# Optimization experiments

Measured on AMD Instinct MI355X. Metric: run time of the kernel, lower is better.

Reference implementation:

```python
import jax, jax.numpy as jnp
import numpy as np

EMB_DIM = 1024
HEAD_NUM = 16
HEAD_DIM = EMB_DIM // HEAD_NUM
B, S = 2, 2048


def setup_inputs() -> dict:
    key = jax.random.key(0)
    k_x, k_wqkv, k_bqkv, k_wo, k_bo = jax.random.split(key, 5)
    x = jax.random.normal(k_x, (B, S, EMB_DIM), dtype=jnp.float32)
    # nn.Linear default init scale ~ 1/sqrt(fan_in); exact distribution irrelevant for a reference
    lim = 1.0 / np.sqrt(EMB_DIM)
    W_qkv = jax.random.uniform(k_wqkv, (EMB_DIM, 3 * EMB_DIM), jnp.float32, -lim, lim)
    b_qkv = jax.random.uniform(k_bqkv, (3 * EMB_DIM,), jnp.float32, -lim, lim)
    W_o = jax.random.uniform(k_wo, (EMB_DIM, EMB_DIM), jnp.float32, -lim, lim)
    b_o = jax.random.uniform(k_bo, (EMB_DIM,), jnp.float32, -lim, lim)
    mask = jnp.tril(jnp.ones((S, S), dtype=bool))  # causal mask as in casual_mask(seq_len)
    return {"x": x, "W_qkv": W_qkv, "b_qkv": b_qkv, "W_o": W_o, "b_o": b_o, "mask": mask}


def reference(x, W_qkv, b_qkv, W_o, b_o, mask):
    b, s, e = x.shape
    qkv = x @ W_qkv + b_qkv                      # [b, s, 3e]
    q, k, v = qkv[..., :e], qkv[..., e:2 * e], qkv[..., 2 * e:]
    # [b, s, h, d] -> [b, h, s, d]
    q = q.reshape(b, s, HEAD_NUM, HEAD_DIM).transpose(0, 2, 1, 3)
    k = k.reshape(b, s, HEAD_NUM, HEAD_DIM).transpose(0, 2, 1, 3)
    v = v.reshape(b, s, HEAD_NUM, HEAD_DIM).transpose(0, 2, 1, 3)
    scores = jnp.einsum("bhqd,bhkd->bhqk", q, k) / jnp.sqrt(jnp.float32(HEAD_DIM))
    scores = jnp.where(mask, scores, -jnp.inf)   # masked_fill(~mask, -inf)
    probs = jax.nn.softmax(scores, axis=-1)      # dropout is identity in eval mode
    out = jnp.einsum("bhqk,bhkd->bhqd", probs, v)
    out = out.transpose(0, 2, 1, 3).reshape(b, s, e)
    return out @ W_o + b_o
```

## Files before the change

### kernel.cpp

```cpp
#include <hip/hip_runtime.h>


typedef __attribute__((ext_vector_type(8))) short short8;
typedef __attribute__((ext_vector_type(4))) float floatx4;

#define NB 2
#define SEQ 2048
#define EMB 1024
#define NH 16
#define HD 64
#define M_ROWS (NB * SEQ)
#define N_QKV (3 * EMB)
#define SLOT_F 4160

#define GLL(g, l) __builtin_amdgcn_global_load_lds( \
    (const __attribute__((address_space(1))) void*)(g), \
    (__attribute__((address_space(3))) void*)(l), 16, 0, 0)

static __device__ __forceinline__ unsigned short f2bf(float f) {
    union { float f; unsigned int u; } v; v.f = f;
    unsigned int r = v.u + 0x7FFFu + ((v.u >> 16) & 1u);
    return (unsigned short)(r >> 16);
}

__global__ void x_to_bf16(const float* __restrict__ in, unsigned short* __restrict__ out, int n4) {
    int i = blockIdx.x * blockDim.x + threadIdx.x;
    if (i >= n4) return;
    float4 v = ((const float4*)in)[i];
    unsigned long long p = (unsigned long long)f2bf(v.x)
        | ((unsigned long long)f2bf(v.y) << 16)
        | ((unsigned long long)f2bf(v.z) << 32)
        | ((unsigned long long)f2bf(v.w) << 48);
    ((unsigned long long*)out)[i] = p;
}

__global__ void transpose_f32_bf16(const float* __restrict__ in,
                                   unsigned short* __restrict__ out, int R, int C) {
    __shared__ unsigned short tile[32][33];
    int tx = threadIdx.x, ty = threadIdx.y;
    int c0 = blockIdx.x * 32, r0 = blockIdx.y * 32;
    #pragma unroll
    for (int j = 0; j < 4; ++j)
        tile[ty + j * 8][tx] = f2bf(in[(size_t)(r0 + ty + j * 8) * C + c0 + tx]);
    __syncthreads();
    #pragma unroll
    for (int j = 0; j < 4; ++j)
        out[(size_t)(c0 + ty + j * 8) * R + r0 + tx] = tile[tx][ty + j * 8];
}

__global__ __launch_bounds__(256) void qkv_gemm(
    const unsigned short* __restrict__ A,
    const unsigned short* __restrict__ Bt,
    const float* __restrict__ bias,
    unsigned short* __restrict__ qb, unsigned short* __restrict__ kb,
    unsigned short* __restrict__ vb)
{
    const int K = EMB;
    __shared__ __align__(16) unsigned short As[128 * 32];
    __shared__ __align__(16) unsigned short Bs[128 * 32];
    int t = threadIdx.x;
    int m0 = blockIdx.y * 128;
    int n0 = blockIdx.x * 128;
    int w = t >> 6, lane = t & 63, quad = lane >> 4, lcol = lane & 15;
    int wr = w >> 1, wc = w & 1;

    floatx4 zero = {0.f, 0.f, 0.f, 0.f};
    floatx4 acc[4][4];
    #pragma unroll
    for (int i = 0; i < 4; ++i)
        #pragma unroll
        for (int j = 0; j < 4; ++j) acc[i][j] = zero;

    const unsigned short* a0 = A  + (size_t)(m0 + (t >> 2)) * K + ((t & 3) << 3);
    const unsigned short* b0 = Bt + (size_t)(n0 + (t >> 2)) * K + ((t & 3) << 3);
    unsigned short* la = &As[t << 3];
    unsigned short* lb = &Bs[t << 3];

    for (int k0 = 0; k0 < K; k0 += 32) {
        __syncthreads();
        GLL(a0 + k0, la);
        GLL(a0 + 64 * K + k0, la + 2048);
        GLL(b0 + k0, lb);
        GLL(b0 + 64 * K + k0, lb + 2048);
        __syncthreads();
        short8 af[4], bfm[4];
        #pragma unroll
        for (int i = 0; i < 4; ++i)
            af[i] = *(const short8*)(&As[(wr * 64 + i * 16 + lcol) * 32 + quad * 8]);
        #pragma unroll
        for (int j = 0; j < 4; ++j)
            bfm[j] = *(const short8*)(&Bs[(wc * 64 + j * 16 + lcol) * 32 + quad * 8]);
        #pragma unroll
        for (int i = 0; i < 4; ++i)
            #pragma unroll
            for (int j = 0; j < 4; ++j)
                acc[i][j] = __builtin_amdgcn_mfma_f32_16x16x32_bf16(af[i], bfm[j], acc[i][j], 0, 0, 0);
    }

    #pragma unroll
    for (int i = 0; i < 4; ++i) {
        int m = m0 + wr * 64 + i * 16 + quad * 4;
        int b = m >> 11, s = m & 2047;
        #pragma unroll
        for (int j = 0; j < 4; ++j) {
            int n = n0 + wc * 64 + j * 16 + lcol;
            int which = n >> 10;
            int e = n & 1023;
            int h = e >> 6, d = e & 63;
            float bv = bias[n];
            if (which == 2) {
                size_t base = ((size_t)((b * NH + h) * HD + d)) * SEQ + s;
                unsigned long long pk = (unsigned long long)f2bf(acc[i][j][0] + bv)
                    | ((unsigned long long)f2bf(acc[i][j][1] + bv) << 16)
                    | ((unsigned long long)f2bf(acc[i][j][2] + bv) << 32)
                    | ((unsigned long long)f2bf(acc[i][j][3] + bv) << 48);
                *(unsigned long long*)(&vb[base]) = pk;
            } else {
                unsigned short* dst = (which == 0) ? qb : kb;
                size_t base = ((size_t)((b * NH + h) * SEQ + s)) * HD + d;
                #pragma unroll
                for (int r = 0; r < 4; ++r)
                    dst[base + (size_t)r * HD] = f2bf(acc[i][j][r] + bv);
            }
        }
    }
}

#define PST 68

__global__ __launch_bounds__(256) void attn_partial(
    const unsigned short* __restrict__ Q,
    const unsigned short* __restrict__ Kk,
    const unsigned short* __restrict__ Vt,
    unsigned short* __restrict__ Out,
    float* __restrict__ Part)
{
    __shared__ __align__(16) unsigned short Ks[2][64 * 64];
    __shared__ __align__(16) unsigned short Vs[2][64 * 64];
    __shared__ __align__(16) unsigned short Ps[4][16 * PST];

    int u = blockIdx.x;
    int bh = blockIdx.y;
    int qt, c;
    if (u < 16) { qt = u; c = 0; }
    else { int v = u - 16; qt = 16 + (v >> 1); c = v & 1; }
    int ktBeg = c << 4;
    int ktEnd = (c == 0 && qt >= 16) ? 16 : (qt + 1);

    int q0 = qt * 64;
    int t = threadIdx.x;
    int w = t >> 6, lane = t & 63, quad = lane >> 4, lcol = lane & 15;
    const size_t hoff = (size_t)bh * SEQ * HD;
    const float SC = 0.18033688011112043f;

    const unsigned short* qp = Q + hoff + (size_t)(q0 + 16 * w + lcol) * HD + quad * 8;
    short8 aq0 = *(const short8*)qp, aq1 = *(const short8*)(qp + 32);

    int srow = t >> 3;
    int ss   = (t & 7) ^ (srow & 7);
    const unsigned short* kgl = Kk + hoff + (size_t)srow * HD + ss * 8;
    const unsigned short* vgl = Vt + hoff + (size_t)srow * SEQ + ss * 8;
    unsigned short* kld = &Ks[0][t * 8];
    unsigned short* vld = &Vs[0][t * 8];

    floatx4 zero = {0.f, 0.f, 0.f, 0.f};
    floatx4 O[4];
    float l[4] = {0.f, 0.f, 0.f, 0.f};
    #pragma unroll
    for (int d = 0; d < 4; ++d) O[d] = zero;

    {
        int k0 = ktBeg * 64;
        GLL(kgl + (size_t)k0 * HD, kld);
        GLL(kgl + (size_t)(k0 + 32) * HD, kld + 2048);
        GLL(vgl + k0, vld);
        GLL(vgl + (size_t)32 * SEQ + k0, vld + 2048);
    }

    int sx0 = (quad ^ (lcol & 7)) << 3;
    int sx1 = sx0 ^ 32;

    for (int kt = ktBeg; kt < ktEnd; ++kt) {
        int cur = kt & 1, nxt = cur ^ 1;
        __syncthreads();
        if (kt + 1 < ktEnd) {
            int k0 = (kt + 1) * 64;
            GLL(kgl + (size_t)k0 * HD, kld + nxt * 4096);
            GLL(kgl + (size_t)(k0 + 32) * HD, kld + nxt * 4096 + 2048);
            GLL(vgl + k0, vld + nxt * 4096);
            GLL(vgl + (size_t)32 * SEQ + k0, vld + nxt * 4096 + 2048);
        }

        const unsigned short* ksr = &Ks[cur][0];
        const unsigned short* vsr = &Vs[cur][0];
        short8 bk0[4], bk1[4], bv0[4], bv1[4];
        #pragma unroll
        for (int tc = 0; tc < 4; ++tc) {
            int rb = (tc * 16 + lcol) << 6;
            bk0[tc] = *(const short8*)(ksr + rb + sx0);
            bk1[tc] = *(const short8*)(ksr + rb + sx1);
            bv0[tc] = *(const short8*)(vsr + rb + sx0);
            bv1[tc] = *(const short8*)(vsr + rb + sx1);
        }

        floatx4 sacc[4];
        #pragma unroll
        for (int tc = 0; tc < 4; ++tc) {
            sacc[tc] = __builtin_amdgcn_mfma_f32_16x16x32_bf16(aq0, bk0[tc], zero, 0, 0, 0);
            sacc[tc] = __builtin_amdgcn_mfma_f32_16x16x32_bf16(aq1, bk1[tc], sacc[tc], 0, 0, 0);
        }
        bool diag = (kt == qt);
        unsigned short* PsW = &Ps[w][0];
        int rbase = 16 * w + quad * 4;
        #pragma unroll
        for (int tc = 0; tc < 4; ++tc) {
            int keyc = tc * 16 + lcol;
            #pragma unroll
            for (int r = 0; r < 4; ++r) {
                float p = __builtin_amdgcn_exp2f(sacc[tc][r] * SC);
                if (diag && keyc > rbase + r) p = 0.f;
                l[r] += p;
                PsW[(quad * 4 + r) * PST + keyc] = f2bf(p);
            }
        }
        short8 ap0 = *(const short8*)(&PsW[lcol * PST + quad * 8]);
        short8 ap1 = *(const short8*)(&PsW[lcol * PST + 32 + quad * 8]);
        #pragma unroll
        for (int td = 0; td < 4; ++td) {
            O[td] = __builtin_amdgcn_mfma_f32_16x16x32_bf16(ap0, bv0[td], O[td], 0, 0, 0);
            O[td] = __builtin_amdgcn_mfma_f32_16x16x32_bf16(ap1, bv1[td], O[td], 0, 0, 0);
        }
    }

    #pragma unroll
    for (int r = 0; r < 4; ++r) {
        #pragma unroll
        for (int off = 1; off < 16; off <<= 1)
            l[r] += __shfl_xor(l[r], off, 64);
    }

    if (qt < 16) {
        int b = bh >> 4, h = bh & 15;
        size_t obase = ((size_t)b * SEQ) * EMB + (size_t)h * HD;
        #pragma unroll
        for (int td = 0; td < 4; ++td) {
            #pragma unroll
            for (int r = 0; r < 4; ++r) {
                int row = q0 + 16 * w + quad * 4 + r;
                Out[obase + (size_t)row * EMB + td * 16 + lcol] = f2bf(O[td][r] / l[r]);
            }
        }
    } else {
        float* slot = Part + ((size_t)(bh * 16 + (qt - 16)) * 2 + c) * SLOT_F;
        #pragma unroll
        for (int td = 0; td < 4; ++td) {
            #pragma unroll
            for (int r = 0; r < 4; ++r)
                slot[(16 * w + quad * 4 + r) * 64 + td * 16 + lcol] = O[td][r];
        }
        if (lcol == 0) {
            #pragma unroll
            for (int r = 0; r < 4; ++r)
                slot[4096 + 16 * w + quad * 4 + r] = l[r];
        }
    }
}

__global__ __launch_bounds__(256) void attn_combine(
    const float* __restrict__ Part, unsigned short* __restrict__ Out)
{
    int qh = blockIdx.x;
    int bh = blockIdx.y;
    int qt = 16 + qh;
    const float* s0 = Part + ((size_t)(bh * 16 + qh) * 2) * SLOT_F;
    const float* s1 = s0 + SLOT_F;
    int b = bh >> 4, h = bh & 15;
    size_t obase = ((size_t)b * SEQ + qt * 64) * EMB + (size_t)h * HD;
    int t = threadIdx.x;
    #pragma unroll
    for (int it = 0; it < 16; ++it) {
        int idx = it * 256 + t;
        int row = idx >> 6, col = idx & 63;
        float lv = s0[4096 + row] + s1[4096 + row];
        float v = (s0[idx] + s1[idx]) / lv;
        Out[obase + (size_t)row * EMB + col] = f2bf(v);
    }
}

__global__ __launch_bounds__(256) void oproj_gemm(
    const unsigned short* __restrict__ A,
    const unsigned short* __restrict__ Bt,
    const float* __restrict__ bias,
    float* __restrict__ Cout)
{
    const int K = EMB;
    __shared__ __align__(16) unsigned short As[128 * 32];
    __shared__ __align__(16) unsigned short Bs[128 * 32];
    int t = threadIdx.x;
    int m0 = blockIdx.y * 128;
    int n0 = blockIdx.x * 128;
    int w = t >> 6, lane = t & 63, quad = lane >> 4, lcol = lane & 15;
    int wr = w >> 1, wc = w & 1;

    floatx4 zero = {0.f, 0.f, 0.f, 0.f};
    floatx4 acc[4][4];
    #pragma unroll
    for (int i = 0; i < 4; ++i)
        #pragma unroll
        for (int j = 0; j < 4; ++j) acc[i][j] = zero;

    const unsigned short* a0 = A  + (size_t)(m0 + (t >> 2)) * K + ((t & 3) << 3);
    const unsigned short* b0 = Bt + (size_t)(n0 + (t >> 2)) * K + ((t & 3) << 3);
    unsigned short* la = &As[t << 3];
    unsigned short* lb = &Bs[t << 3];

    for (int k0 = 0; k0 < K; k0 += 32) {
        __syncthreads();
        GLL(a0 + k0, la);
        GLL(a0 + 64 * K + k0, la + 2048);
        GLL(b0 + k0, lb);
        GLL(b0 + 64 * K + k0, lb + 2048);
        __syncthreads();
        short8 af[4], bfm[4];
        #pragma unroll
        for (int i = 0; i < 4; ++i)
            af[i] = *(const short8*)(&As[(wr * 64 + i * 16 + lcol) * 32 + quad * 8]);
        #pragma unroll
        for (int j = 0; j < 4; ++j)
            bfm[j] = *(const short8*)(&Bs[(wc * 64 + j * 16 + lcol) * 32 + quad * 8]);
        #pragma unroll
        for (int i = 0; i < 4; ++i)
            #pragma unroll
            for (int j = 0; j < 4; ++j)
                acc[i][j] = __builtin_amdgcn_mfma_f32_16x16x32_bf16(af[i], bfm[j], acc[i][j], 0, 0, 0);
    }

    #pragma unroll
    for (int i = 0; i < 4; ++i) {
        int m = m0 + wr * 64 + i * 16 + quad * 4;
        #pragma unroll
        for (int j = 0; j < 4; ++j) {
            int n = n0 + wc * 64 + j * 16 + lcol;
            float bv = bias[n];
            #pragma unroll
            for (int r = 0; r < 4; ++r)
                Cout[(size_t)(m + r) * EMB + n] = acc[i][j][r] + bv;
        }
    }
}

extern "C" void kernel_launch(void* const* d_in, const int* in_sizes, int n_in,
                              void* d_out, int out_size, void* d_ws, size_t ws_size,
                              hipStream_t stream) {
    (void)in_sizes; (void)n_in; (void)out_size; (void)ws_size;
    char* ws = (char*)d_ws;
    const size_t OFF_X     = 0;
    const size_t OFF_WQKVT = OFF_X     + (size_t)M_ROWS * EMB * 2;
    const size_t OFF_WOT   = OFF_WQKVT + (size_t)N_QKV * EMB * 2;
    const size_t OFF_Q     = OFF_WOT   + (size_t)EMB * EMB * 2;
    const size_t OFF_K     = OFF_Q     + (size_t)M_ROWS * EMB * 2;
    const size_t OFF_V     = OFF_K     + (size_t)M_ROWS * EMB * 2;
    const size_t OFF_ATTN  = OFF_V     + (size_t)M_ROWS * EMB * 2;
    const size_t OFF_PART  = OFF_ATTN  + (size_t)M_ROWS * EMB * 2;

    const float* x    = (const float*)d_in[0];
    const float* Wqkv = (const float*)d_in[1];
    const float* bqkv = (const float*)d_in[2];
    const float* Wo   = (const float*)d_in[3];
    const float* bo   = (const float*)d_in[4];

    unsigned short* x_bf  = (unsigned short*)(ws + OFF_X);
    unsigned short* wqkvT = (unsigned short*)(ws + OFF_WQKVT);
    unsigned short* woT   = (unsigned short*)(ws + OFF_WOT);
    unsigned short* qb    = (unsigned short*)(ws + OFF_Q);
    unsigned short* kb    = (unsigned short*)(ws + OFF_K);
    unsigned short* vb    = (unsigned short*)(ws + OFF_V);
    unsigned short* attn  = (unsigned short*)(ws + OFF_ATTN);
    float*          part  = (float*)(ws + OFF_PART);

    x_to_bf16<<<(M_ROWS * EMB / 4 + 255) / 256, 256, 0, stream>>>(x, x_bf, M_ROWS * EMB / 4);
    transpose_f32_bf16<<<dim3(N_QKV / 32, EMB / 32), dim3(32, 8), 0, stream>>>(Wqkv, wqkvT, EMB, N_QKV);
    transpose_f32_bf16<<<dim3(EMB / 32, EMB / 32), dim3(32, 8), 0, stream>>>(Wo, woT, EMB, EMB);

    qkv_gemm<<<dim3(N_QKV / 128, M_ROWS / 128), 256, 0, stream>>>(x_bf, wqkvT, bqkv, qb, kb, vb);
    attn_partial<<<dim3(48, NB * NH), 256, 0, stream>>>(qb, kb, vb, attn, part);
    attn_combine<<<dim3(16, NB * NH), 256, 0, stream>>>(part, attn);
    oproj_gemm<<<dim3(EMB / 128, M_ROWS / 128), 256, 0, stream>>>(attn, woT, bo, (float*)d_out);
}
```

Measured before the change: 241.9 us.

## Stage QKV GEMM epilogue through LDS for coalesced 16-byte stores; split diagonal softmax path

```diff
diff --git a/kernel.cpp b/kernel.cpp
--- a/kernel.cpp
+++ b/kernel.cpp
@@ -48,6 +48,8 @@
         out[(size_t)(c0 + ty + j * 8) * R + r0 + tx] = tile[tx][ty + j * 8];
 }
 
+#define CTS 130
+
 __global__ __launch_bounds__(256) void qkv_gemm(
     const unsigned short* __restrict__ A,
     const unsigned short* __restrict__ Bt,
@@ -56,8 +58,10 @@
     unsigned short* __restrict__ vb)
 {
     const int K = EMB;
-    __shared__ __align__(16) unsigned short As[128 * 32];
-    __shared__ __align__(16) unsigned short Bs[128 * 32];
+    __shared__ __align__(16) unsigned short smem[128 * CTS];
+    unsigned short* As = smem;
+    unsigned short* Bs = smem + 4096;
+
     int t = threadIdx.x;
     int m0 = blockIdx.y * 128;
     int n0 = blockIdx.x * 128;
@@ -97,31 +101,48 @@
                 acc[i][j] = __builtin_amdgcn_mfma_f32_16x16x32_bf16(af[i], bfm[j], acc[i][j], 0, 0, 0);
     }
 
+    bool isV = (n0 >= 2 * EMB);
+    __syncthreads();
     #pragma unroll
     for (int i = 0; i < 4; ++i) {
-        int m = m0 + wr * 64 + i * 16 + quad * 4;
-        int b = m >> 11, s = m & 2047;
+        int row0 = wr * 64 + i * 16 + quad * 4;
         #pragma unroll
         for (int j = 0; j < 4; ++j) {
-            int n = n0 + wc * 64 + j * 16 + lcol;
-            int which = n >> 10;
-            int e = n & 1023;
-            int h = e >> 6, d = e & 63;
-            float bv = bias[n];
-            if (which == 2) {
-                size_t base = ((size_t)((b * NH + h) * HD + d)) * SEQ + s;
-                unsigned long long pk = (unsigned long long)f2bf(acc[i][j][0] + bv)
-                    | ((unsigned long long)f2bf(acc[i][j][1] + bv) << 16)
-                    | ((unsigned long long)f2bf(acc[i][j][2] + bv) << 32)
-                    | ((unsigned long long)f2bf(acc[i][j][3] + bv) << 48);
-                *(unsigned long long*)(&vb[base]) = pk;
-            } else {
-                unsigned short* dst = (which == 0) ? qb : kb;
-                size_t base = ((size_t)((b * NH + h) * SEQ + s)) * HD + d;
-                #pragma unroll
-                for (int r = 0; r < 4; ++r)
-                    dst[base + (size_t)r * HD] = f2bf(acc[i][j][r] + bv);
+            int col = wc * 64 + j * 16 + lcol;
+            float bv = bias[n0 + col];
+            #pragma unroll
+            for (int r = 0; r < 4; ++r) {
+                unsigned short hv = f2bf(acc[i][j][r] + bv);
+                if (isV) smem[col * CTS + row0 + r] = hv;
+                else     smem[(row0 + r) * CTS + col] = hv;
             }
+        }
+    }
+    __syncthreads();
+
+    int b = m0 >> 11, s0 = m0 & 2047;
+    int hbase = (n0 & 1023) >> 6;
+    if (!isV) {
+        unsigned short* dst = (n0 >= EMB) ? kb : qb;
+        #pragma unroll
+        for (int it = 0; it < 8; ++it) {
+            int job = it * 32 + (t >> 3);
+            int tok = job & 127, hh = job >> 7;
+            int chunk = t & 7;
+            short8 vv = *(const short8*)(&smem[tok * CTS + hh * 64 + chunk * 8]);
+            size_t g = ((size_t)((b * NH + hbase + hh) * SEQ + s0 + tok)) * HD + chunk * 8;
+            *(short8*)(&dst[g]) = vv;
+        }
+    } else {
+        #pragma unroll
+        for (int it = 0; it < 8; ++it) {
+            int job = it * 32 + (t >> 3);
+            int f = job & 127, half = job >> 7;
+            int chunk = (t & 7) + half * 8;
+            short8 vv = *(const short8*)(&smem[f * CTS + chunk * 8]);
+            int h = hbase + (f >> 6), d = f & 63;
+            size_t g = ((size_t)((b * NH + h) * HD + d)) * SEQ + s0 + chunk * 8;
+            *(short8*)(&vb[g]) = vv;
         }
     }
 }
@@ -209,18 +230,30 @@
             sacc[tc] = __builtin_amdgcn_mfma_f32_16x16x32_bf16(aq0, bk0[tc], zero, 0, 0, 0);
             sacc[tc] = __builtin_amdgcn_mfma_f32_16x16x32_bf16(aq1, bk1[tc], sacc[tc], 0, 0, 0);
         }
-        bool diag = (kt == qt);
         unsigned short* PsW = &Ps[w][0];
-        int rbase = 16 * w + quad * 4;
-        #pragma unroll
-        for (int tc = 0; tc < 4; ++tc) {
-            int keyc = tc * 16 + lcol;
-            #pragma unroll
-            for (int r = 0; r < 4; ++r) {
-                float p = __builtin_amdgcn_exp2f(sacc[tc][r] * SC);
-                if (diag && keyc > rbase + r) p = 0.f;
-                l[r] += p;
-                PsW[(quad * 4 + r) * PST + keyc] = f2bf(p);
+        if (kt == qt) {
+            int rbase = 16 * w + quad * 4;
+            #pragma unroll
+            for (int tc = 0; tc < 4; ++tc) {
+                int keyc = tc * 16 + lcol;
+                #pragma unroll
+                for (int r = 0; r < 4; ++r) {
+                    float p = __builtin_amdgcn_exp2f(sacc[tc][r] * SC);
+                    if (keyc > rbase + r) p = 0.f;
+                    l[r] += p;
+                    PsW[(quad * 4 + r) * PST + keyc] = f2bf(p);
+                }
+            }
+        } else {
+            #pragma unroll
+            for (int tc = 0; tc < 4; ++tc) {
+                int keyc = tc * 16 + lcol;
+                #pragma unroll
+                for (int r = 0; r < 4; ++r) {
+                    float p = __builtin_amdgcn_exp2f(sacc[tc][r] * SC);
+                    l[r] += p;
+                    PsW[(quad * 4 + r) * PST + keyc] = f2bf(p);
+                }
             }
         }
         short8 ap0 = *(const short8*)(&PsW[lcol * PST + quad * 8]);
```

After: 224.6 us. 1.08x faster.
